# Kernel tuning notes

Hardware: AMD Instinct MI355X
Metric: run time of the kernel (lower is better)

## Reference

```python
import jax, jax.numpy as jnp
import numpy as np

N, F, NEWF = 8192, 128, 64
NEG_INF = -1e10
LEAKY_ALPHA = 0.2


def setup_inputs() -> dict:
    key = jax.random.key(0)
    k1, k2, k3, k4, k5 = jax.random.split(key, 5)
    X = jax.random.normal(k1, (N, F), dtype=jnp.float32)
    A = jax.random.randint(k2, (N, N), 0, 2, dtype=jnp.int32)
    W = jax.random.normal(k3, (F, NEWF), dtype=jnp.float32) * (1.0 / np.sqrt(F))
    a_self = jax.random.normal(k4, (NEWF, 1), dtype=jnp.float32) * (1.0 / np.sqrt(NEWF))
    a_neigh = jax.random.normal(k5, (NEWF, 1), dtype=jnp.float32) * (1.0 / np.sqrt(NEWF))
    return {"X": X, "A": A, "W": W, "a_self": a_self, "a_neigh": a_neigh}


def reference(X, A, W, a_self, a_neigh):
    # Linear transform: [N, newF]
    h = X @ W
    # Additive attention logits: self_attn[i] + neigh_attn[j] -> [N, N]
    self_attn = h @ a_self      # [N, 1]
    neigh_attn = h @ a_neigh    # [N, 1]
    dense = self_attn + neigh_attn.T               # [N, N]
    dense = jax.nn.leaky_relu(dense, LEAKY_ALPHA)
    # Mask: -1e10 where A == 0, else 0
    masked = jnp.where(A == 0, dense + NEG_INF, dense)
    attn = jax.nn.softmax(masked, axis=-1)
    # Dropout is identity at inference (Keras Dropout without training=True)
    out = attn @ h                                  # [N, newF]
    return jax.nn.relu(out)
```

## Files before the change

### kernel.cpp

```cpp
#include <hip/hip_runtime.h>

#define N 8192
#define F 128
#define NEWF 64
#define ALPHA 0.2f
#define JSPLIT 8
#define JW (N / JSPLIT)
#define RB 64
#define PIECE 128
#define NPIECE (JW / PIECE)

typedef float f32x4 __attribute__((ext_vector_type(4)));
typedef short short8 __attribute__((ext_vector_type(8)));

typedef const __attribute__((address_space(1))) unsigned* gp_t;
typedef __attribute__((address_space(3))) unsigned* lp_t;
static __device__ __forceinline__ void gload_lds16(const void* g, void* l) {
    __builtin_amdgcn_global_load_lds((gp_t)g, (lp_t)l, 16, 0, 0);
}

__global__ void k_hsn(const float* __restrict__ X, const float* __restrict__ W,
                      const float* __restrict__ a_self, const float* __restrict__ a_neigh,
                      float* __restrict__ h, float* __restrict__ s, float* __restrict__ n) {
    int row = blockIdx.x * 4 + (threadIdx.x >> 6);
    int l = threadIdx.x & 63;
    const float* xr = X + (size_t)row * F;
    float acc = 0.0f;
#pragma unroll 8
    for (int f = 0; f < F; ++f) acc += xr[f] * W[f * NEWF + l];
    h[(size_t)row * NEWF + l] = acc;
    float ts = acc * a_self[l];
    float tn = acc * a_neigh[l];
#pragma unroll
    for (int off = 32; off; off >>= 1) {
        ts += __shfl_xor(ts, off);
        tn += __shfl_xor(tn, off);
    }
    if (l == 0) { s[row] = ts; n[row] = tn; }
}

__global__ void k_tr(const float* __restrict__ h, unsigned short* __restrict__ hThi,
                     unsigned short* __restrict__ hTlo) {
    __shared__ float tile[64][65];
    const int t = threadIdx.x;
    const int j0 = blockIdx.x * 64;
    {
        const int jr = t >> 2, cs = (t & 3) * 16;
        const float4* src = (const float4*)(h + (size_t)(j0 + jr) * NEWF + cs);
#pragma unroll
        for (int q = 0; q < 4; ++q) {
            float4 v = src[q];
            tile[jr][cs + q * 4 + 0] = v.x; tile[jr][cs + q * 4 + 1] = v.y;
            tile[jr][cs + q * 4 + 2] = v.z; tile[jr][cs + q * 4 + 3] = v.w;
        }
    }
    __syncthreads();
    {
        const int c = t >> 2, js = (t & 3) * 16;
        short8 hi0 = {}, hi1 = {}, lo0 = {}, lo1 = {};
#pragma unroll
        for (int k = 0; k < 16; ++k) {
            float v = tile[js + k][c];
            unsigned xb = __float_as_uint(v);
            short hb = (short)(xb >> 16);
            float lof = v - __uint_as_float(xb & 0xffff0000u);
            short lb = (short)(__float_as_uint(lof) >> 16);
            if (k < 8) { hi0[k] = hb; lo0[k] = lb; }
            else       { hi1[k - 8] = hb; lo1[k - 8] = lb; }
        }
        size_t off = (size_t)c * N + j0 + js;
        *(short8*)(hThi + off)     = hi0;
        *(short8*)(hThi + off + 8) = hi1;
        *(short8*)(hTlo + off)     = lo0;
        *(short8*)(hTlo + off + 8) = lo1;
    }
}

__global__ void k_nmax(const float* __restrict__ n, float* __restrict__ nmax) {
    __shared__ float red[1024];
    int t = threadIdx.x;
    float4 v0 = ((const float4*)n)[t];
    float4 v1 = ((const float4*)n)[t + 1024];
    float m = fmaxf(fmaxf(fmaxf(v0.x, v0.y), fmaxf(v0.z, v0.w)),
                    fmaxf(fmaxf(v1.x, v1.y), fmaxf(v1.z, v1.w)));
    red[t] = m;
    __syncthreads();
    for (int off = 512; off; off >>= 1) {
        if (t < off) red[t] = fmaxf(red[t], red[t + off]);
        __syncthreads();
    }
    if (t == 0) nmax[0] = red[0];
}

__global__ void __launch_bounds__(256, 4) k_main(
        const int* __restrict__ A, const float* __restrict__ s,
        const float* __restrict__ n, const float* __restrict__ nmaxp,
        const unsigned short* __restrict__ hThi, const unsigned short* __restrict__ hTlo,
        float* __restrict__ pacc, float* __restrict__ pz) {
    __shared__ __align__(16) unsigned short slab[16384];

    const int tid = threadIdx.x;
    const int w = tid >> 6, l = tid & 63;
    const int lr = l & 15, lg = l >> 4;

    const int rb = blockIdx.x / JSPLIT;
    const int js = blockIdx.x % JSPLIT;
    const int r0 = rb * RB + w * 16;
    const int jb = js * JW;

    const float sval = s[r0 + lr];
    const float tM = sval + nmaxp[0];
    const float Mv = fmaxf(tM, ALPHA * tM);
    float zacc = 0.0f;

    f32x4 acc0 = {0.f,0.f,0.f,0.f}, acc1 = {0.f,0.f,0.f,0.f};
    f32x4 acc2 = {0.f,0.f,0.f,0.f}, acc3 = {0.f,0.f,0.f,0.f};

    const int sr_lo = tid >> 4;
    const int s_jsh = (((tid & 15) * 16) ^ ((sr_lo & 7) << 4)) >> 1;
    char* slabc = (char*)slab;
    const int rswz = (lr & 7) << 4;

#define STAGE(piece)                                                          \
    {                                                                         \
        const size_t gcol = (size_t)jb + (size_t)(piece) * PIECE + s_jsh;     \
        _Pragma("unroll")                                                     \
        for (int q = 0; q < 8; ++q) {                                         \
            const int r_ = (q & 3) * 16 + sr_lo;                              \
            const unsigned short* gp_ =                                       \
                ((q >> 2) ? hTlo : hThi) + (size_t)r_ * N + gcol;             \
            gload_lds16(gp_, slabc + q * 4096 + tid * 16);                    \
        }                                                                     \
    }

    const int4*   Ap  = (const int4*)(A + (size_t)(r0 + lr) * N + jb + lg * 8);
    const float4* npv = (const float4*)(n + jb + lg * 8);

    STAGE(0);
    int4 a0 = Ap[0], a1 = Ap[1];
    float4 nv0 = npv[0], nv1 = npv[1];
    asm volatile("s_waitcnt vmcnt(0)" ::: "memory");
    __builtin_amdgcn_s_barrier();
    __builtin_amdgcn_sched_barrier(0);

    for (int piece = 0; piece < NPIECE; ++piece) {
#pragma unroll
        for (int k = 0; k < 4; ++k) {
            const int ci = piece * 4 + k;
            const int cn = (ci + 1 < NPIECE * 4) ? ci + 1 : 0;

            int4 na0 = Ap[(size_t)cn * 8], na1 = Ap[(size_t)cn * 8 + 1];
            float4 nn0 = npv[(size_t)cn * 8], nn1 = npv[(size_t)cn * 8 + 1];
            __builtin_amdgcn_sched_barrier(0);

            int   av[8] = {a0.x, a0.y, a0.z, a0.w, a1.x, a1.y, a1.z, a1.w};
            float nf[8] = {nv0.x, nv0.y, nv0.z, nv0.w, nv1.x, nv1.y, nv1.z, nv1.w};
            short8 ahi, alo;
#pragma unroll
            for (int j = 0; j < 8; ++j) {
                float t  = sval + nf[j];
                float lv = fmaxf(t, ALPHA * t);
                float ex = __expf(lv - Mv);
                ex = (av[j] != 0) ? ex : 0.0f;
                zacc += ex;
                unsigned xb = __float_as_uint(ex);
                ahi[j] = (short)(xb >> 16);
                float lof = ex - __uint_as_float(xb & 0xffff0000u);
                alo[j] = (short)(__float_as_uint(lof) >> 16);
            }

            const int joff = (k * 64 + lg * 16) ^ rswz;
            const char* rp = (const char*)slab + lr * 256 + joff;
            short8 B0h = *(const short8*)(rp);
            short8 B1h = *(const short8*)(rp + 16 * 256);
            short8 B2h = *(const short8*)(rp + 32 * 256);
            short8 B3h = *(const short8*)(rp + 48 * 256);
            short8 B0l = *(const short8*)(rp + 16384);
            short8 B1l = *(const short8*)(rp + 16384 + 16 * 256);
            short8 B2l = *(const short8*)(rp + 16384 + 32 * 256);
            short8 B3l = *(const short8*)(rp + 16384 + 48 * 256);

            acc0 = __builtin_amdgcn_mfma_f32_16x16x32_bf16(ahi, B0h, acc0, 0, 0, 0);
            acc1 = __builtin_amdgcn_mfma_f32_16x16x32_bf16(ahi, B1h, acc1, 0, 0, 0);
            acc2 = __builtin_amdgcn_mfma_f32_16x16x32_bf16(ahi, B2h, acc2, 0, 0, 0);
            acc3 = __builtin_amdgcn_mfma_f32_16x16x32_bf16(ahi, B3h, acc3, 0, 0, 0);
            acc0 = __builtin_amdgcn_mfma_f32_16x16x32_bf16(ahi, B0l, acc0, 0, 0, 0);
            acc1 = __builtin_amdgcn_mfma_f32_16x16x32_bf16(ahi, B1l, acc1, 0, 0, 0);
            acc2 = __builtin_amdgcn_mfma_f32_16x16x32_bf16(ahi, B2l, acc2, 0, 0, 0);
            acc3 = __builtin_amdgcn_mfma_f32_16x16x32_bf16(ahi, B3l, acc3, 0, 0, 0);
            acc0 = __builtin_amdgcn_mfma_f32_16x16x32_bf16(alo, B0h, acc0, 0, 0, 0);
            acc1 = __builtin_amdgcn_mfma_f32_16x16x32_bf16(alo, B1h, acc1, 0, 0, 0);
            acc2 = __builtin_amdgcn_mfma_f32_16x16x32_bf16(alo, B2h, acc2, 0, 0, 0);
            acc3 = __builtin_amdgcn_mfma_f32_16x16x32_bf16(alo, B3h, acc3, 0, 0, 0);

            a0 = na0; a1 = na1; nv0 = nn0; nv1 = nn1;
        }

        if (piece + 1 < NPIECE) {
            __builtin_amdgcn_s_barrier();
            __builtin_amdgcn_sched_barrier(0);
            STAGE(piece + 1);
            asm volatile("s_waitcnt vmcnt(0)" ::: "memory");
            __builtin_amdgcn_s_barrier();
            __builtin_amdgcn_sched_barrier(0);
        }
    }
#undef STAGE

    zacc += __shfl_xor(zacc, 16);
    zacc += __shfl_xor(zacc, 32);

    float* pa = pacc + ((size_t)js * N + r0) * NEWF;
#pragma unroll
    for (int r = 0; r < 4; ++r) {
        int row = lg * 4 + r;
        pa[(size_t)row * NEWF +  0 + lr] = acc0[r];
        pa[(size_t)row * NEWF + 16 + lr] = acc1[r];
        pa[(size_t)row * NEWF + 32 + lr] = acc2[r];
        pa[(size_t)row * NEWF + 48 + lr] = acc3[r];
    }
    if (l < 16) pz[(size_t)js * N + r0 + lr] = zacc;
}

__global__ void k_fin(const float* __restrict__ pacc, const float* __restrict__ pz,
                      float* __restrict__ out) {
    int t = blockIdx.x * 256 + threadIdx.x;
    int i = t >> 6, k = t & 63;
    float v = 0.0f, z = 0.0f;
#pragma unroll
    for (int psl = 0; psl < JSPLIT; ++psl) {
        v += pacc[((size_t)psl * N + i) * NEWF + k];
        z += pz[(size_t)psl * N + i];
    }
    out[t] = fmaxf(v / z, 0.0f);
}

extern "C" void kernel_launch(void* const* d_in, const int* in_sizes, int n_in,
                              void* d_out, int out_size, void* d_ws, size_t ws_size,
                              hipStream_t stream) {
    const float* X       = (const float*)d_in[0];
    const int*   A       = (const int*)d_in[1];
    const float* W       = (const float*)d_in[2];
    const float* a_self  = (const float*)d_in[3];
    const float* a_neigh = (const float*)d_in[4];
    float* out = (float*)d_out;

    float* wsf = (float*)d_ws;
    float* h    = wsf;
    float* s    = h + (size_t)N * NEWF;
    float* nv   = s + N;
    float* nmax = nv + N;
    unsigned short* hThi = (unsigned short*)(nmax + 4);
    unsigned short* hTlo = hThi + (size_t)N * NEWF;
    float* pacc = (float*)(hTlo + (size_t)N * NEWF);
    float* pz   = pacc + (size_t)JSPLIT * N * NEWF;

    k_hsn <<<N / 4,        256, 0, stream>>>(X, W, a_self, a_neigh, h, s, nv);
    k_tr  <<<N / 64,       256, 0, stream>>>(h, hThi, hTlo);
    k_nmax<<<1,           1024, 0, stream>>>(nv, nmax);
    k_main<<<(N / RB) * JSPLIT, 256, 0, stream>>>(A, s, nv, nmax, hThi, hTlo, pacc, pz);
    k_fin <<<(N * NEWF) / 256, 256, 0, stream>>>(pacc, pz, out);
}
```

Measured before the change: 425.1 us.

## Stage adjacency mask and h tiles through double-buffered async LDS pipeline

The adjacency matrix A and the neighbour logits n now go into LDS through async global_load_lds copies, alongside the split hT tiles. Before, A was read straight into registers with a one-chunk register prefetch. The LDS tiles are double-buffered with 64-column pieces, and vmcnt-based waits let the load of piece p+1 overlap compute on piece p. The column split drops from 8 to 4 blocks per row band, which halves partial-sum traffic and k_fin work. The cost is a 72KB LDS footprint and launch bounds lowered to 2 blocks per CU, so occupancy falls and latency hiding depends more on the explicit pipeline.

```diff
diff --git a/kernel.cpp b/kernel.cpp
--- a/kernel.cpp
+++ b/kernel.cpp
@@ -4,11 +4,11 @@
 #define F 128
 #define NEWF 64
 #define ALPHA 0.2f
-#define JSPLIT 8
+#define JSPLIT 4
 #define JW (N / JSPLIT)
 #define RB 64
-#define PIECE 128
-#define NPIECE (JW / PIECE)
+#define PIECE 64
+#define NP (JW / PIECE)
 
 typedef float f32x4 __attribute__((ext_vector_type(4)));
 typedef short short8 __attribute__((ext_vector_type(8)));
@@ -92,119 +92,139 @@
     if (t == 0) nmax[0] = red[0];
 }
 
-__global__ void __launch_bounds__(256, 4) k_main(
-        const int* __restrict__ A, const float* __restrict__ s,
+__global__ void __launch_bounds__(256, 2) k_main(
+        const int* __restrict__ Araw, const float* __restrict__ s,
         const float* __restrict__ n, const float* __restrict__ nmaxp,
         const unsigned short* __restrict__ hThi, const unsigned short* __restrict__ hTlo,
         float* __restrict__ pacc, float* __restrict__ pz) {
-    __shared__ __align__(16) unsigned short slab[16384];
+    __shared__ __align__(16) char lds[73728];
 
     const int tid = threadIdx.x;
     const int w = tid >> 6, l = tid & 63;
     const int lr = l & 15, lg = l >> 4;
 
-    const int rb = blockIdx.x / JSPLIT;
-    const int js = blockIdx.x % JSPLIT;
-    const int r0 = rb * RB + w * 16;
+    const int rbk = blockIdx.x / JSPLIT;
+    const int js  = blockIdx.x % JSPLIT;
+    const int rblk = rbk * RB;
+    const int r0 = rblk + w * 16;
     const int jb = js * JW;
 
+    f32x4 acc0 = {0.f,0.f,0.f,0.f}, acc1 = {0.f,0.f,0.f,0.f};
+    f32x4 acc2 = {0.f,0.f,0.f,0.f}, acc3 = {0.f,0.f,0.f,0.f};
+    float zacc = 0.0f;
+
+#define STAGE(piece, b)                                                        \
+    {                                                                          \
+        char* Ad = lds + (b) * 16384;                                          \
+        char* Bd = lds + 32768 + (b) * 16384;                                  \
+        const int jp = jb + (piece) * PIECE;                                   \
+        _Pragma("unroll")                                                      \
+        for (int q = 0; q < 4; ++q) {                                          \
+            const int arw = q * 16 + (tid >> 4);                               \
+            const int acol = ((tid & 15) * 16) ^ ((arw & 7) << 4);             \
+            gload_lds16(Araw + (size_t)(rblk + arw) * N + jp + (acol >> 2),    \
+                        Ad + q * 4096 + tid * 16);                             \
+        }                                                                      \
+        _Pragma("unroll")                                                      \
+        for (int q = 0; q < 4; ++q) {                                          \
+            const int brw = (q & 1) * 32 + (tid >> 3);                         \
+            const int bcol = ((tid & 7) * 16) ^ ((brw & 7) << 4);              \
+            const unsigned short* srcb =                                       \
+                ((q >> 1) ? hTlo : hThi) + (size_t)brw * N + jp + (bcol >> 1); \
+            gload_lds16(srcb, Bd + q * 4096 + tid * 16);                       \
+        }                                                                      \
+    }
+
+#define CHUNK(p_, b_, ch_)                                                     \
+    {                                                                          \
+        const char* Ab = lds + (b_) * 16384;                                   \
+        const char* Bb = lds + 32768 + (b_) * 16384;                           \
+        const float* nsl = (const float*)(lds + 65536);                        \
+        const int swz = (lr & 7) << 4;                                         \
+        const int arow = w * 16 + lr;                                          \
+        const int acol = (ch_) * 128 + lg * 32;                                \
+        int4 av0 = *(const int4*)(Ab + arow * 256 + (acol ^ swz));             \
+        int4 av1 = *(const int4*)(Ab + arow * 256 + ((acol + 16) ^ swz));      \
+        const float* np0 = nsl + ((p_) * PIECE + (ch_) * 32 + lg * 8);         \
+        float4 nv0 = *(const float4*)(np0);                                    \
+        float4 nv1 = *(const float4*)(np0 + 4);                                \
+        int   av[8] = {av0.x, av0.y, av0.z, av0.w, av1.x, av1.y, av1.z, av1.w};\
+        float nf[8] = {nv0.x, nv0.y, nv0.z, nv0.w, nv1.x, nv1.y, nv1.z, nv1.w};\
+        short8 ahi, alo;                                                       \
+        _Pragma("unroll")                                                      \
+        for (int j = 0; j < 8; ++j) {                                          \
+            float t  = sval + nf[j];                                           \
+            float lv = fmaxf(t, ALPHA * t);                                    \
+            float ex = __expf(lv - Mv);                                        \
+            ex = (av[j] != 0) ? ex : 0.0f;                                     \
+            zacc += ex;                                                        \
+            unsigned xb = __float_as_uint(ex);                                 \
+            ahi[j] = (short)(xb >> 16);                                        \
+            float lof = ex - __uint_as_float(xb & 0xffff0000u);                \
+            alo[j] = (short)(__float_as_uint(lof) >> 16);                      \
+        }                                                                      \
+        const int bcol = ((ch_) * 64 + lg * 16) ^ swz;                         \
+        short8 B0h = *(const short8*)(Bb + (lr +  0) * 128 + bcol);            \
+        short8 B1h = *(const short8*)(Bb + (lr + 16) * 128 + bcol);            \
+        short8 B2h = *(const short8*)(Bb + (lr + 32) * 128 + bcol);            \
+        short8 B3h = *(const short8*)(Bb + (lr + 48) * 128 + bcol);            \
+        short8 B0l = *(const short8*)(Bb + 8192 + (lr +  0) * 128 + bcol);     \
+        short8 B1l = *(const short8*)(Bb + 8192 + (lr + 16) * 128 + bcol);     \
+        short8 B2l = *(const short8*)(Bb + 8192 + (lr + 32) * 128 + bcol);     \
+        short8 B3l = *(const short8*)(Bb + 8192 + (lr + 48) * 128 + bcol);     \
+        acc0 = __builtin_amdgcn_mfma_f32_16x16x32_bf16(ahi, B0h, acc0, 0, 0, 0);\
+        acc1 = __builtin_amdgcn_mfma_f32_16x16x32_bf16(ahi, B1h, acc1, 0, 0, 0);\
+        acc2 = __builtin_amdgcn_mfma_f32_16x16x32_bf16(ahi, B2h, acc2, 0, 0, 0);\
+        acc3 = __builtin_amdgcn_mfma_f32_16x16x32_bf16(ahi, B3h, acc3, 0, 0, 0);\
+        acc0 = __builtin_amdgcn_mfma_f32_16x16x32_bf16(ahi, B0l, acc0, 0, 0, 0);\
+        acc1 = __builtin_amdgcn_mfma_f32_16x16x32_bf16(ahi, B1l, acc1, 0, 0, 0);\
+        acc2 = __builtin_amdgcn_mfma_f32_16x16x32_bf16(ahi, B2l, acc2, 0, 0, 0);\
+        acc3 = __builtin_amdgcn_mfma_f32_16x16x32_bf16(ahi, B3l, acc3, 0, 0, 0);\
+        acc0 = __builtin_amdgcn_mfma_f32_16x16x32_bf16(alo, B0h, acc0, 0, 0, 0);\
+        acc1 = __builtin_amdgcn_mfma_f32_16x16x32_bf16(alo, B1h, acc1, 0, 0, 0);\
+        acc2 = __builtin_amdgcn_mfma_f32_16x16x32_bf16(alo, B2h, acc2, 0, 0, 0);\
+        acc3 = __builtin_amdgcn_mfma_f32_16x16x32_bf16(alo, B3h, acc3, 0, 0, 0);\
+    }
+
+#define COMPUTE(p_, b_) { CHUNK(p_, b_, 0); CHUNK(p_, b_, 1); }
+
+    gload_lds16(n + jb + tid * 4,        lds + 65536 + tid * 16);
+    gload_lds16(n + jb + 1024 + tid * 4, lds + 65536 + 4096 + tid * 16);
+    STAGE(0, 0);
+    STAGE(1, 1);
     const float sval = s[r0 + lr];
     const float tM = sval + nmaxp[0];
     const float Mv = fmaxf(tM, ALPHA * tM);
-    float zacc = 0.0f;
-
-    f32x4 acc0 = {0.f,0.f,0.f,0.f}, acc1 = {0.f,0.f,0.f,0.f};
-    f32x4 acc2 = {0.f,0.f,0.f,0.f}, acc3 = {0.f,0.f,0.f,0.f};
-
-    const int sr_lo = tid >> 4;
-    const int s_jsh = (((tid & 15) * 16) ^ ((sr_lo & 7) << 4)) >> 1;
-    char* slabc = (char*)slab;
-    const int rswz = (lr & 7) << 4;
-
-#define STAGE(piece)                                                          \
-    {                                                                         \
-        const size_t gcol = (size_t)jb + (size_t)(piece) * PIECE + s_jsh;     \
-        _Pragma("unroll")                                                     \
-        for (int q = 0; q < 8; ++q) {                                         \
-            const int r_ = (q & 3) * 16 + sr_lo;                              \
-            const unsigned short* gp_ =                                       \
-                ((q >> 2) ? hTlo : hThi) + (size_t)r_ * N + gcol;             \
-            gload_lds16(gp_, slabc + q * 4096 + tid * 16);                    \
-        }                                                                     \
-    }
-
-    const int4*   Ap  = (const int4*)(A + (size_t)(r0 + lr) * N + jb + lg * 8);
-    const float4* npv = (const float4*)(n + jb + lg * 8);
-
-    STAGE(0);
-    int4 a0 = Ap[0], a1 = Ap[1];
-    float4 nv0 = npv[0], nv1 = npv[1];
+
     asm volatile("s_waitcnt vmcnt(0)" ::: "memory");
+    __builtin_amdgcn_sched_barrier(0);
     __builtin_amdgcn_s_barrier();
     __builtin_amdgcn_sched_barrier(0);
 
-    for (int piece = 0; piece < NPIECE; ++piece) {
-#pragma unroll
-        for (int k = 0; k < 4; ++k) {
-            const int ci = piece * 4 + k;
-            const int cn = (ci + 1 < NPIECE * 4) ? ci + 1 : 0;
-
-            int4 na0 = Ap[(size_t)cn * 8], na1 = Ap[(size_t)cn * 8 + 1];
-            float4 nn0 = npv[(size_t)cn * 8], nn1 = npv[(size_t)cn * 8 + 1];
-            __builtin_amdgcn_sched_barrier(0);
-
-            int   av[8] = {a0.x, a0.y, a0.z, a0.w, a1.x, a1.y, a1.z, a1.w};
-            float nf[8] = {nv0.x, nv0.y, nv0.z, nv0.w, nv1.x, nv1.y, nv1.z, nv1.w};
-            short8 ahi, alo;
-#pragma unroll
-            for (int j = 0; j < 8; ++j) {
-                float t  = sval + nf[j];
-                float lv = fmaxf(t, ALPHA * t);
-                float ex = __expf(lv - Mv);
-                ex = (av[j] != 0) ? ex : 0.0f;
-                zacc += ex;
-                unsigned xb = __float_as_uint(ex);
-                ahi[j] = (short)(xb >> 16);
-                float lof = ex - __uint_as_float(xb & 0xffff0000u);
-                alo[j] = (short)(__float_as_uint(lof) >> 16);
-            }
-
-            const int joff = (k * 64 + lg * 16) ^ rswz;
-            const char* rp = (const char*)slab + lr * 256 + joff;
-            short8 B0h = *(const short8*)(rp);
-            short8 B1h = *(const short8*)(rp + 16 * 256);
-            short8 B2h = *(const short8*)(rp + 32 * 256);
-            short8 B3h = *(const short8*)(rp + 48 * 256);
-            short8 B0l = *(const short8*)(rp + 16384);
-            short8 B1l = *(const short8*)(rp + 16384 + 16 * 256);
-            short8 B2l = *(const short8*)(rp + 16384 + 32 * 256);
-            short8 B3l = *(const short8*)(rp + 16384 + 48 * 256);
-
-            acc0 = __builtin_amdgcn_mfma_f32_16x16x32_bf16(ahi, B0h, acc0, 0, 0, 0);
-            acc1 = __builtin_amdgcn_mfma_f32_16x16x32_bf16(ahi, B1h, acc1, 0, 0, 0);
-            acc2 = __builtin_amdgcn_mfma_f32_16x16x32_bf16(ahi, B2h, acc2, 0, 0, 0);
-            acc3 = __builtin_amdgcn_mfma_f32_16x16x32_bf16(ahi, B3h, acc3, 0, 0, 0);
-            acc0 = __builtin_amdgcn_mfma_f32_16x16x32_bf16(ahi, B0l, acc0, 0, 0, 0);
-            acc1 = __builtin_amdgcn_mfma_f32_16x16x32_bf16(ahi, B1l, acc1, 0, 0, 0);
-            acc2 = __builtin_amdgcn_mfma_f32_16x16x32_bf16(ahi, B2l, acc2, 0, 0, 0);
-            acc3 = __builtin_amdgcn_mfma_f32_16x16x32_bf16(ahi, B3l, acc3, 0, 0, 0);
-            acc0 = __builtin_amdgcn_mfma_f32_16x16x32_bf16(alo, B0h, acc0, 0, 0, 0);
-            acc1 = __builtin_amdgcn_mfma_f32_16x16x32_bf16(alo, B1h, acc1, 0, 0, 0);
-            acc2 = __builtin_amdgcn_mfma_f32_16x16x32_bf16(alo, B2h, acc2, 0, 0, 0);
-            acc3 = __builtin_amdgcn_mfma_f32_16x16x32_bf16(alo, B3h, acc3, 0, 0, 0);
-
-            a0 = na0; a1 = na1; nv0 = nn0; nv1 = nn1;
-        }
-
-        if (piece + 1 < NPIECE) {
-            __builtin_amdgcn_s_barrier();
-            __builtin_amdgcn_sched_barrier(0);
-            STAGE(piece + 1);
-            asm volatile("s_waitcnt vmcnt(0)" ::: "memory");
-            __builtin_amdgcn_s_barrier();
-            __builtin_amdgcn_sched_barrier(0);
-        }
-    }
+    COMPUTE(0, 0);
+    __builtin_amdgcn_s_barrier();
+    __builtin_amdgcn_sched_barrier(0);
+    STAGE(2, 0);
+
+    for (int p = 1; p < NP - 1; ++p) {
+        asm volatile("s_waitcnt vmcnt(8)" ::: "memory");
+        __builtin_amdgcn_sched_barrier(0);
+        __builtin_amdgcn_s_barrier();
+        __builtin_amdgcn_sched_barrier(0);
+        COMPUTE(p, p & 1);
+        __builtin_amdgcn_s_barrier();
+        __builtin_amdgcn_sched_barrier(0);
+        if (p < NP - 2) STAGE(p + 2, p & 1);
+    }
+
+    asm volatile("s_waitcnt vmcnt(0)" ::: "memory");
+    __builtin_amdgcn_sched_barrier(0);
+    __builtin_amdgcn_s_barrier();
+    __builtin_amdgcn_sched_barrier(0);
+    COMPUTE(NP - 1, (NP - 1) & 1);
+
+#undef COMPUTE
+#undef CHUNK
 #undef STAGE
 
     zacc += __shfl_xor(zacc, 16);
```

After: 420.1 us. Within noise of the previous version (-1.2%).
